# Kernel tuning notes

Hardware: AMD Instinct MI355X
Metric: run time of the kernel (lower is better)

Reference implementation:

```python
import jax, jax.numpy as jnp
import numpy as np

N = 8192          # nodes (atoms)
E = N * 20        # edges (avg 20 neighbors)
NG = 32           # graphs in batch
CUTOFF = 10.0
NBASIS = 40
NNEI = 20.0       # num_neighbors normalization
SQ2 = 0.5 ** 0.5


def _swish(x):
    return x * jax.nn.sigmoid(x)


def _radial(r, params):
    # Gaussian radial basis on [0, cutoff] followed by swish MLP 40->500->500->50->nweight
    centers = jnp.linspace(0.0, CUTOFF, NBASIS)
    width = centers[1] - centers[0]
    x = jnp.exp(-(((r[:, None] - centers) / width) ** 2))  # [E, NBASIS]
    w1, b1, w2, b2, w3, b3, w4, b4 = params
    x = _swish(x @ w1 + b1)
    x = _swish(x @ w2 + b2)
    x = _swish(x @ w3 + b3)
    return x @ w4 + b4


def setup_inputs() -> dict:
    key = jax.random.key(0)
    ks = jax.random.split(key, 12)
    z = jax.random.randint(ks[0], (N,), 0, 100)
    pos = jax.random.normal(ks[1], (N, 3), dtype=jnp.float32) * 2.0
    batch = jnp.sort(jax.random.randint(ks[2], (N,), 0, NG))
    edge_index = jax.random.randint(ks[3], (2, E), 0, N)

    def mlp_params(kk, dout):
        dims = [NBASIS, 500, 500, 50, dout]
        keys = jax.random.split(kk, len(dims) - 1)
        out = []
        for i, (a, b) in enumerate(zip(dims[:-1], dims[1:])):
            out.append(jax.random.normal(keys[i], (a, b), jnp.float32) / jnp.sqrt(a))
            out.append(jnp.zeros((b,), jnp.float32))
        return out

    rm1 = mlp_params(ks[4], 30 * 40 + 30 * 10)  # tp weights: 0x0->0 and 0x1->1 paths
    rm2 = mlp_params(ks[5], 30 * 1 + 10 * 1)    # tp weights: 0x0->0 and 1x1->0 paths
    inp = {
        'pos': pos,
        'emb': jax.random.normal(ks[6], (100, 30), jnp.float32),
        'si1_w': jax.random.normal(ks[7], (30, 40), jnp.float32),
        'si2_w': jax.random.normal(ks[8], (30, 1), jnp.float32),
    }
    names1 = ['rm1_w1', 'rm1_b1', 'rm1_w2', 'rm1_b2', 'rm1_w3', 'rm1_b3', 'rm1_w4', 'rm1_b4']
    names2 = ['rm2_w1', 'rm2_b1', 'rm2_w2', 'rm2_b2', 'rm2_w3', 'rm2_b3', 'rm2_w4', 'rm2_b4']
    inp.update(dict(zip(names1, rm1)))
    inp.update(dict(zip(names2, rm2)))
    inp['z'] = z
    inp['edge_index'] = edge_index
    inp['batch'] = batch
    return inp


def _forward(pos, emb, si1_w, si2_w, rm1, rm2, z, edge_index, batch):
    n = pos.shape[0]
    h = emb[z]                                  # [N, 30] embedding of atomic number
    row, col = edge_index[0], edge_index[1]
    edge_vec = pos[row] - pos[col]              # [E, 3]
    r = jnp.sqrt(jnp.sum(edge_vec ** 2, axis=1) + 1e-12)
    unit = edge_vec / r[:, None]
    # spherical harmonics (component norm): l=0 -> 1, l=1 -> sqrt(3)*unit; scaled by 1/sqrt(num_neighbors)
    sh = jnp.concatenate([jnp.ones_like(r)[:, None], jnp.sqrt(3.0) * unit], 1) / jnp.sqrt(NNEI)  # [E,4]
    e = edge_vec.shape[0]

    # ---- layer 1 Conv: (30,0,+) -> (40,0,+) + (10,1,-) ----
    s = h @ si1_w / jnp.sqrt(30.0)                                   # self-interaction, scalar block
    s_full = jnp.concatenate([s, jnp.zeros((n, 30), s.dtype)], 1)    # l=1 block has no input -> 0
    w = _radial(r, rm1)                                              # [E, 1500] per-edge tp weights
    w00 = w[:, :1200].reshape(e, 30, 40)
    w01 = w[:, 1200:].reshape(e, 30, 10)
    xj = h[row]
    m0 = jnp.einsum('eu,euv->ev', xj, w00) * sh[:, :1] / jnp.sqrt(30.0)                        # [E,40]
    m1 = jnp.einsum('eu,euv->ev', xj, w01)[:, :, None] * sh[:, None, 1:4] / jnp.sqrt(30.0)     # [E,10,3]
    msg = jnp.concatenate([m0, m1.reshape(e, 30)], 1)                # [E,70]
    agg = jax.ops.segment_sum(msg, col, num_segments=n)
    mask1 = jnp.concatenate([jnp.ones(40), jnp.zeros(30)]).astype(h.dtype)  # si output mask
    h1 = SQ2 * s_full + (1.0 + (SQ2 - 1.0) * mask1) * agg            # [N,70]

    # ---- gated block: swish on scalars, sigmoid gates on l=1 vectors ----
    scalars = _swish(h1[:, :30])
    gates = jax.nn.sigmoid(h1[:, 30:40])
    nons = h1[:, 40:70].reshape(n, 10, 3) * gates[:, :, None]
    h2 = jnp.concatenate([scalars, nons.reshape(n, 30)], 1)          # [N,60]

    # ---- final Conv: (30,0,+)+(10,1,-) -> (1,0,+)+(1,0,-) ----
    s2 = h2[:, :30] @ si2_w / jnp.sqrt(30.0)                         # [N,1]
    s2_full = jnp.concatenate([s2, jnp.zeros((n, 1), s2.dtype)], 1)
    w2 = _radial(r, rm2)                                             # [E,40]
    xj2 = h2[row]
    m0a = jnp.sum(xj2[:, :30] * w2[:, :30], axis=1) * sh[:, 0] / jnp.sqrt(30.0)
    dot = jnp.einsum('eum,em->eu', xj2[:, 30:].reshape(e, 10, 3), sh[:, 1:4]) / jnp.sqrt(3.0)  # 1x1->0 CG
    m0b = jnp.sum(dot * w2[:, 30:40], axis=1) / jnp.sqrt(10.0)
    msg2 = jnp.stack([m0a + m0b, jnp.zeros_like(m0a)], 1)            # (0,-1) output has no tp path
    agg2 = jax.ops.segment_sum(msg2, col, num_segments=n)
    mask2 = jnp.array([1.0, 0.0], h.dtype)
    hf = SQ2 * s2_full + (1.0 + (SQ2 - 1.0) * mask2) * agg2
    node_out = hf[:, 0] + hf[:, 1] ** 2
    return jax.ops.segment_sum(node_out[:, None], batch, num_segments=NG)  # [NG, 1]


def reference(pos, emb, si1_w, si2_w, rm1_w1, rm1_b1, rm1_w2, rm1_b2, rm1_w3, rm1_b3, rm1_w4, rm1_b4, rm2_w1, rm2_b1, rm2_w2, rm2_b2, rm2_w3, rm2_b3, rm2_w4, rm2_b4, z, edge_index, batch):
    rm1 = (rm1_w1, rm1_b1, rm1_w2, rm1_b2, rm1_w3, rm1_b3, rm1_w4, rm1_b4)
    rm2 = (rm2_w1, rm2_b1, rm2_w2, rm2_b2, rm2_w3, rm2_b3, rm2_w4, rm2_b4)
    return _forward(pos, emb, si1_w, si2_w, rm1, rm2, z, edge_index, batch)
```

## Files before the change

### kernel.cpp

```cpp
#include <hip/hip_runtime.h>
#include <stdint.h>

typedef __attribute__((ext_vector_type(8))) short bf16x8;
typedef __attribute__((ext_vector_type(4))) float f32x4;

#define N_NODES 8192
#define E_EDGES 163840
#define NGRAPH  32

#define INV_SQRT30 0.18257419f
#define SH0C       0.22360680f
#define SQRT3C     1.73205081f
#define INV_SQRT3  0.57735027f
#define INV_SQRT10 0.31622777f
#define SQ2C       0.70710678f

enum : unsigned {
  OFF_W1P1 = 0u,       OFF_W2P1 = 65536u,   OFF_W3P1 = 589824u,  OFF_W4P1 = 655360u,
  OFF_W1P2 = 851968u,  OFF_W2P2 = 917504u,  OFF_W3P2 = 1441792u, OFF_W4P2 = 1507328u,
  OFF_B1P1 = 1515520u, OFF_B2P1 = 1517568u, OFF_B3P1 = 1519616u, OFF_B4P1 = 1519872u,
  OFF_B1P2 = 1526016u, OFF_B2P2 = 1528064u, OFF_B3P2 = 1530112u, OFF_B4P2 = 1530368u,
  OFF_HN   = 1530624u,
  OFF_H2   = 2579200u,
  OFF_AGG  = 4676352u,
  OFF_AGG2 = 6970112u,
  OFF_GSUM = 7002880u,
  OFF_ZEND = 7003008u,
  OFF_SHL  = 7003136u,
  OFF_BAS  = 8969216u,
  OFF_W4N1 = 29940736u,
  OFF_X3   = 30186496u
};

__device__ __forceinline__ uint16_t f2bf(float f){
  union { float f; uint32_t u; } v; v.f = f;
  uint32_t r = v.u + 0x7fffu + ((v.u >> 16) & 1u);
  return (uint16_t)(r >> 16);
}
__device__ __forceinline__ float swishf(float x){ return x / (1.f + __expf(-x)); }
__device__ __forceinline__ float swish_fast(float x){
  float d = 1.f + __expf(-x);
  return x * __builtin_amdgcn_rcpf(d);
}

__device__ __forceinline__ void pack_mat(const float* __restrict__ src, int K, int N, int NP,
                                         uint16_t* __restrict__ dst, int t)
{
  int lane = t & 63;
  int tile = t >> 6;
  int NT = NP >> 4;
  int nn = tile % NT, kk = tile / NT;
  int k0 = kk*32 + ((lane >> 4) << 3);
  int n  = nn*16 + (lane & 15);
  union { short s[8]; bf16x8 v; } tmp;
#pragma unroll
  for (int b = 0; b < 8; ++b) {
    int k = k0 + b;
    tmp.s[b] = (k < K && n < N) ? (short)f2bf(src[(size_t)k*N + n]) : (short)0;
  }
  *reinterpret_cast<bf16x8*>(dst + (size_t)t*8) = tmp.v;
}

__device__ __forceinline__ void pack_w4n(const float* __restrict__ w4, const float* __restrict__ b4,
                                         uint16_t* __restrict__ dst, int t)
{
  int lane = t & 63;
  int tile = t >> 6;
  int u = tile >> 3, j = tile & 7;
  int kk = j >> 2, nn = j & 3;
  int k0 = kk*32 + ((lane >> 4) << 3);
  int n  = nn*16 + (lane & 15);
  union { short s[8]; bf16x8 v; } tmp;
#pragma unroll
  for (int b = 0; b < 8; ++b) {
    int k = k0 + b;
    float val = 0.f;
    if (n < 50) {
      int cg = (n < 40) ? (u*40 + n) : (1200 + u*10 + (n - 40));
      if (k < 50) val = w4[(size_t)k*1500 + cg];
      else if (k == 63) val = b4[cg];
    }
    tmp.s[b] = (short)f2bf(val);
  }
  *reinterpret_cast<bf16x8*>(dst + (size_t)t*8) = tmp.v;
}

__global__ void prep_kernel(const float* w1a, const float* w2a, const float* w3a, const float* w4a,
                            const float* w1b, const float* w2b, const float* w3b, const float* w4b,
                            const float* b1a, const float* b2a, const float* b3a, const float* b4a,
                            const float* b1b, const float* b2b, const float* b3b, const float* b4b,
                            const float* emb, const int* z, char* ws)
{
  int t = blockIdx.x * 256 + threadIdx.x;
  if      (t < 4096)   pack_mat(w1a, 40, 500, 512,  (uint16_t*)(ws + OFF_W1P1), t);
  else if (t < 36864)  pack_mat(w2a, 500,500, 512,  (uint16_t*)(ws + OFF_W2P1), t - 4096);
  else if (t < 40960)  pack_mat(w3a, 500, 50, 64,   (uint16_t*)(ws + OFF_W3P1), t - 36864);
  else if (t < 45056)  {  }
  else if (t < 49152)  pack_mat(w1b, 40, 500, 512,  (uint16_t*)(ws + OFF_W1P2), t - 45056);
  else if (t < 81920)  pack_mat(w2b, 500,500, 512,  (uint16_t*)(ws + OFF_W2P2), t - 49152);
  else if (t < 86016)  pack_mat(w3b, 500, 50, 64,   (uint16_t*)(ws + OFF_W3P2), t - 81920);
  else if (t < 86528)  pack_mat(w4b, 50,  40, 64,   (uint16_t*)(ws + OFF_W4P2), t - 86016);
  else if (t < 90304) {
    int loc = t - 86528;
    const float* src; float* dst; int realN;
    if      (loc < 512)  { src=b1a; dst=(float*)(ws+OFF_B1P1); realN=500; }
    else if (loc < 1024) { src=b2a; dst=(float*)(ws+OFF_B2P1); realN=500;  loc -= 512;  }
    else if (loc < 1088) { src=b3a; dst=(float*)(ws+OFF_B3P1); realN=50;   loc -= 1024; }
    else if (loc < 2624) { src=b4a; dst=(float*)(ws+OFF_B4P1); realN=1500; loc -= 1088; }
    else if (loc < 3136) { src=b1b; dst=(float*)(ws+OFF_B1P2); realN=500;  loc -= 2624; }
    else if (loc < 3648) { src=b2b; dst=(float*)(ws+OFF_B2P2); realN=500;  loc -= 3136; }
    else if (loc < 3712) { src=b3b; dst=(float*)(ws+OFF_B3P2); realN=50;   loc -= 3648; }
    else                 { src=b4b; dst=(float*)(ws+OFF_B4P2); realN=40;   loc -= 3712; }
    dst[loc] = (loc < realN) ? src[loc] : 0.f;
  }
  else if (t < 352448) {
    int i = t - 90304;
    int n = i >> 5, u = i & 31;
    float v = 0.f;
    if (u < 30) v = emb[(size_t)z[n]*30 + u] * INV_SQRT30;
    ((float*)(ws + OFF_HN))[i] = v;
  }
  else if (t < 367808) {
    pack_w4n(w4a, b4a, (uint16_t*)(ws + OFF_W4N1), t - 352448);
  }
}

__global__ void edge_meta(const float* __restrict__ pos, const int* __restrict__ eidx,
                          uint16_t* __restrict__ basis, float* __restrict__ shl)
{
  int e = blockIdx.x * 256 + threadIdx.x;
  if (e >= E_EDGES) return;
  int rn = eidx[e], cn = eidx[E_EDGES + e];
  float ax = pos[rn*3+0] - pos[cn*3+0];
  float ay = pos[rn*3+1] - pos[cn*3+1];
  float az = pos[rn*3+2] - pos[cn*3+2];
  float rr = sqrtf(ax*ax + ay*ay + az*az + 1e-12f);
  float s = SQRT3C * SH0C / rr;
  shl[e*3+0] = ax*s; shl[e*3+1] = ay*s; shl[e*3+2] = az*s;
#pragma unroll
  for (int j = 0; j < 8; ++j) {
    union { short s[8]; bf16x8 v; } tmp;
#pragma unroll
    for (int b = 0; b < 8; ++b) {
      int c = j*8 + b;
      float vv = 0.f;
      if (c < 40) { float t = rr*3.9f - (float)c; vv = __expf(-t*t); }
      tmp.s[b] = (short)f2bf(vv);
    }
    *reinterpret_cast<bf16x8*>(basis + (size_t)e*64 + j*8) = tmp.v;
  }
}

__global__ __launch_bounds__(512, 2)
void fused_mlp(const uint16_t* __restrict__ basis,
               const uint16_t* __restrict__ W1p, const float* __restrict__ b1,
               const uint16_t* __restrict__ W2p, const float* __restrict__ b2,
               const uint16_t* __restrict__ W3p, const float* __restrict__ b3,
               uint16_t* __restrict__ x3)
{
  __shared__ __align__(16) char actb[65536];

  const int tid = threadIdx.x, lane = tid & 63, wv = tid >> 6;
  const int m0 = blockIdx.x * 64;
  const int r = lane & 15, q = lane >> 4;

  const bf16x8* __restrict__ W1v = (const bf16x8*)W1p;
  const bf16x8* __restrict__ W2v = (const bf16x8*)W2p;
  const bf16x8* __restrict__ W3v = (const bf16x8*)W3p;

  f32x4 zv = {0.f, 0.f, 0.f, 0.f};
  const int colb2 = (wv*64 + r)*2;

  {
    f32x4 acc[4][4];
#pragma unroll
    for (int a = 0; a < 4; ++a)
#pragma unroll
      for (int c = 0; c < 4; ++c) acc[a][c] = zv;
#pragma unroll
    for (int ks = 0; ks < 2; ++ks) {
      bf16x8 af[4];
#pragma unroll
      for (int rb = 0; rb < 4; ++rb) {
        int row = m0 + rb*16 + r;
        af[rb] = *reinterpret_cast<const bf16x8*>((const char*)basis + (size_t)row*128 + ks*64 + q*16);
      }
      bf16x8 bfr[4];
#pragma unroll
      for (int j = 0; j < 4; ++j)
        bfr[j] = W1v[(size_t)((ks*32 + wv*4 + j)*64 + lane)];
#pragma unroll
      for (int j = 0; j < 4; ++j)
#pragma unroll
        for (int rb = 0; rb < 4; ++rb)
          acc[rb][j] = __builtin_amdgcn_mfma_f32_16x16x32_bf16(af[rb], bfr[j], acc[rb][j], 0, 0, 0);
    }
    float bsv[4];
#pragma unroll
    for (int nt = 0; nt < 4; ++nt) bsv[nt] = b1[wv*64 + nt*16 + r];
#pragma unroll
    for (int rb = 0; rb < 4; ++rb)
#pragma unroll
      for (int i = 0; i < 4; ++i) {
        int row = rb*16 + q*4 + i;
        int rowbase = row*1024;
        int mask = (row & 7) << 4;
#pragma unroll
        for (int nt = 0; nt < 4; ++nt)
          *(uint16_t*)(&actb[rowbase + ((colb2 + nt*32) ^ mask)]) = f2bf(swish_fast(acc[rb][nt][i] + bsv[nt]));
      }
  }
  __syncthreads();

  {
    f32x4 acc[4][4];
#pragma unroll
    for (int a = 0; a < 4; ++a)
#pragma unroll
      for (int c = 0; c < 4; ++c) acc[a][c] = zv;

    bf16x8 bnx[4];
#pragma unroll
    for (int j = 0; j < 4; ++j)
      bnx[j] = W2v[(size_t)((wv*4 + j)*64 + lane)];

#pragma unroll 1
    for (int ks = 0; ks < 16; ++ks) {
      bf16x8 bcur[4];
#pragma unroll
      for (int j = 0; j < 4; ++j) bcur[j] = bnx[j];
      if (ks + 1 < 16) {
#pragma unroll
        for (int j = 0; j < 4; ++j)
          bnx[j] = W2v[(size_t)(((ks + 1)*32 + wv*4 + j)*64 + lane)];
      }
      bf16x8 af[4];
#pragma unroll
      for (int rb = 0; rb < 4; ++rb) {
        int row = rb*16 + r;
        int off = row*1024 + ((ks*64 + q*16) ^ ((row & 7) << 4));
        af[rb] = *reinterpret_cast<const bf16x8*>(&actb[off]);
      }
#pragma unroll
      for (int j = 0; j < 4; ++j)
#pragma unroll
        for (int rb = 0; rb < 4; ++rb)
          acc[rb][j] = __builtin_amdgcn_mfma_f32_16x16x32_bf16(af[rb], bcur[j], acc[rb][j], 0, 0, 0);
    }
    __syncthreads();
    float bsv[4];
#pragma unroll
    for (int nt = 0; nt < 4; ++nt) bsv[nt] = b2[wv*64 + nt*16 + r];
#pragma unroll
    for (int rb = 0; rb < 4; ++rb)
#pragma unroll
      for (int i = 0; i < 4; ++i) {
        int row = rb*16 + q*4 + i;
        int rowbase = row*1024;
        int mask = (row & 7) << 4;
#pragma unroll
        for (int nt = 0; nt < 4; ++nt)
          *(uint16_t*)(&actb[rowbase + ((colb2 + nt*32) ^ mask)]) = f2bf(swish_fast(acc[rb][nt][i] + bsv[nt]));
      }
  }
  __syncthreads();

  {
    const int rb3 = wv >> 1, ntp = (wv & 1)*2;
    f32x4 acc[2];
    acc[0] = zv; acc[1] = zv;

    bf16x8 bnx[2];
#pragma unroll
    for (int j = 0; j < 2; ++j)
      bnx[j] = W3v[(size_t)((ntp + j)*64 + lane)];

#pragma unroll 1
    for (int ks = 0; ks < 16; ++ks) {
      bf16x8 bcur[2];
      bcur[0] = bnx[0]; bcur[1] = bnx[1];
      if (ks + 1 < 16) {
#pragma unroll
        for (int j = 0; j < 2; ++j)
          bnx[j] = W3v[(size_t)(((ks + 1)*4 + ntp + j)*64 + lane)];
      }
      int row = rb3*16 + r;
      int off = row*1024 + ((ks*64 + q*16) ^ ((row & 7) << 4));
      bf16x8 a = *reinterpret_cast<const bf16x8*>(&actb[off]);
#pragma unroll
      for (int j = 0; j < 2; ++j)
        acc[j] = __builtin_amdgcn_mfma_f32_16x16x32_bf16(a, bcur[j], acc[j], 0, 0, 0);
    }
#pragma unroll
    for (int j = 0; j < 2; ++j) {
      int col = (ntp + j)*16 + r;
      float bs = b3[col];
#pragma unroll
      for (int i = 0; i < 4; ++i) {
        int row = m0 + rb3*16 + q*4 + i;
        float v = swish_fast(acc[j][i] + bs);
        if (col == 63) v = 1.f;
        x3[(size_t)row*64 + col] = f2bf(v);
      }
    }
  }
}

__global__ __launch_bounds__(512, 4)
void tp1_gemm(const uint16_t* __restrict__ x3, const char* __restrict__ ws,
              const int* __restrict__ eidx, float* __restrict__ agg)
{
  __shared__ __align__(16) uint16_t Wst[2][4096];
  __shared__ float xjs[64*32];
  __shared__ float mbuf[64*64];
  __shared__ float shls[64*3];
  __shared__ int   rowl[64];
  __shared__ int   coll[64];

  const float* hN  = (const float*)(ws + OFF_HN);
  const float* shl = (const float*)(ws + OFF_SHL);
  const char*  W4n = (const char*)(ws + OFF_W4N1);

  const int tid = threadIdx.x, lane = tid & 63, wv = tid >> 6;
  const int e0l = blockIdx.x * 64;
  const int r_ = lane & 15, q_ = lane >> 4;
  const int rowg = wv >> 1, colg = wv & 1;

  if (tid < 64) { rowl[tid] = eidx[e0l + tid]; coll[tid] = eidx[E_EDGES + e0l + tid]; }
  for (int i = tid; i < 192; i += 512) shls[i] = shl[(size_t)e0l*3 + i];
  __syncthreads();
  for (int i = tid; i < 64*32; i += 512) {
    int e = i >> 5, u = i & 31;
    xjs[i] = hN[(size_t)rowl[e]*32 + u];
  }

  bf16x8 a0, a1;
  {
    int row = e0l + rowg*16 + r_;
    const char* base = (const char*)x3 + (size_t)row*128 + q_*16;
    a0 = *reinterpret_cast<const bf16x8*>(base);
    a1 = *reinterpret_cast<const bf16x8*>(base + 64);
  }

  const char* srcW = W4n + ((size_t)(tid >> 6)*64 + lane)*16;
  auto stageW = [&](int buf, int u) {
    __builtin_amdgcn_global_load_lds((const __attribute__((address_space(1))) void*)(srcW + (size_t)u*8192),
        (__attribute__((address_space(3))) void*)(&Wst[buf][(size_t)tid*8]), 16, 0, 0);
  };

  f32x4 zv = {0.f, 0.f, 0.f, 0.f};
  f32x4 accF[2];
  accF[0] = zv; accF[1] = zv;

  stageW(0, 0);
  __syncthreads();

  const char* wb0 = (const char*)&Wst[0][0] + ((size_t)(colg*2)*64 + lane)*16;
  const char* wb1 = (const char*)&Wst[1][0] + ((size_t)(colg*2)*64 + lane)*16;

  int cur = 0;
#pragma unroll 1
  for (int u = 0; u < 30; ++u) {
    if (u + 1 < 30) stageW(cur ^ 1, u + 1);
    const char* wb = cur ? wb1 : wb0;
    bf16x8 b00 = *reinterpret_cast<const bf16x8*>(wb);
    bf16x8 b01 = *reinterpret_cast<const bf16x8*>(wb + 1024);
    bf16x8 b10 = *reinterpret_cast<const bf16x8*>(wb + 4096);
    bf16x8 b11 = *reinterpret_cast<const bf16x8*>(wb + 5120);
    f32x4 t0 = __builtin_amdgcn_mfma_f32_16x16x32_bf16(a0, b00, zv, 0, 0, 0);
    t0 = __builtin_amdgcn_mfma_f32_16x16x32_bf16(a1, b10, t0, 0, 0, 0);
    f32x4 t1 = __builtin_amdgcn_mfma_f32_16x16x32_bf16(a0, b01, zv, 0, 0, 0);
    t1 = __builtin_amdgcn_mfma_f32_16x16x32_bf16(a1, b11, t1, 0, 0, 0);
#pragma unroll
    for (int i = 0; i < 4; ++i) {
      float xv = xjs[(rowg*16 + q_*4 + i)*32 + u];
      accF[0][i] += xv * t0[i];
      accF[1][i] += xv * t1[i];
    }
    if (u + 1 < 30) {
      asm volatile("s_waitcnt vmcnt(0)" ::: "memory");
      __builtin_amdgcn_s_barrier();
      cur ^= 1;
    }
  }

#pragma unroll
  for (int nt = 0; nt < 2; ++nt)
#pragma unroll
    for (int i = 0; i < 4; ++i)
      mbuf[(rowg*16 + q_*4 + i)*64 + colg*32 + nt*16 + r_] = accF[nt][i];
  __syncthreads();

#pragma unroll 1
  for (int i = tid; i < 64*70; i += 512) {
    int e = i/70, c = i - e*70;
    float v;
    if (c < 40) v = mbuf[e*64 + c] * SH0C;
    else { int vv = (c - 40)/3, k = (c - 40) - vv*3; v = mbuf[e*64 + 40 + vv] * shls[e*3 + k]; }
    atomicAdd(&agg[(size_t)coll[e]*70 + c], v);
  }
}

__global__ __launch_bounds__(512, 2)
void tp2_kernel(const uint16_t* __restrict__ x3, const char* __restrict__ ws,
                const int* __restrict__ eidx, float* __restrict__ agg2)
{
  constexpr int P2 = 67;
  __shared__ float wbuf2[64 * P2];
  __shared__ float xjs[64*30];
  __shared__ float xjv[64*30];
  __shared__ float Db[64*10];
  __shared__ float shls[64*3];
  __shared__ int   rowl[64];
  __shared__ int   coll[64];

  const float* h2  = (const float*)(ws + OFF_H2);
  const float* shl = (const float*)(ws + OFF_SHL);
  const float* b4p = (const float*)(ws + OFF_B4P2);
  const bf16x8* __restrict__ bv4 = (const bf16x8*)(ws + OFF_W4P2);

  const int tid = threadIdx.x, lane = tid & 63, wv = tid >> 6;
  const int e0l = blockIdx.x * 64;
  const int r_ = lane & 15, q_ = lane >> 4;

  if (tid < 64) { rowl[tid] = eidx[e0l + tid]; coll[tid] = eidx[E_EDGES + e0l + tid]; }
  for (int i = tid; i < 192; i += 512) shls[i] = shl[(size_t)e0l*3 + i];
  __syncthreads();
  for (int i = tid; i < 64*60; i += 512) {
    int e = i/60, u = i - e*60;
    float v = h2[(size_t)rowl[e]*64 + u];
    if (u < 30) xjs[e*30 + u] = v; else xjv[e*30 + (u - 30)] = v;
  }
  __syncthreads();
  for (int i = tid; i < 640; i += 512) {
    int e = i/10, v = i - e*10;
    float d = 0.f;
#pragma unroll
    for (int m = 0; m < 3; ++m) d += xjv[e*30 + v*3 + m] * shls[e*3 + m];
    Db[i] = d * INV_SQRT3;
  }

  const int rbase = (wv >> 2)*2, nt4 = wv & 3;
  bf16x8 a4[2][2];
#pragma unroll
  for (int kk = 0; kk < 2; ++kk)
#pragma unroll
    for (int rbi = 0; rbi < 2; ++rbi) {
      int row = e0l + (rbase + rbi)*16 + r_;
      a4[kk][rbi] = *reinterpret_cast<const bf16x8*>((const char*)x3 + (size_t)row*128 + kk*64 + q_*16);
    }
  f32x4 acc[2];
  f32x4 zv = {0.f, 0.f, 0.f, 0.f};
  acc[0] = zv; acc[1] = zv;
#pragma unroll
  for (int kk = 0; kk < 2; ++kk) {
    bf16x8 b4 = bv4[(size_t)(kk*4 + nt4)*64 + lane];
#pragma unroll
    for (int rbi = 0; rbi < 2; ++rbi)
      acc[rbi] = __builtin_amdgcn_mfma_f32_16x16x32_bf16(a4[kk][rbi], b4, acc[rbi], 0, 0, 0);
  }
  __syncthreads();
  {
    int cg = nt4*16 + r_;
    float bs = b4p[cg];
#pragma unroll
    for (int rbi = 0; rbi < 2; ++rbi)
#pragma unroll
      for (int i2 = 0; i2 < 4; ++i2) {
        int e = (rbase + rbi)*16 + q_*4 + i2;
        wbuf2[e*P2 + cg] = acc[rbi][i2] + bs;
      }
  }
  __syncthreads();

  if (tid < 64) {
    int e = tid;
    float m = 0.f, m2 = 0.f;
#pragma unroll
    for (int c = 0; c < 30; ++c) m += xjs[e*30 + c] * wbuf2[e*P2 + c];
#pragma unroll
    for (int vv = 0; vv < 10; ++vv) m2 += Db[e*10 + vv] * wbuf2[e*P2 + 30 + vv];
    atomicAdd(&agg2[coll[e]], m * (SH0C * INV_SQRT30) + m2 * INV_SQRT10);
  }
}

__global__ void node_mid(char* ws, const float* __restrict__ si1w)
{
  int nid = blockIdx.x * blockDim.x + threadIdx.x;
  if (nid >= N_NODES) return;
  const float* hN  = (const float*)(ws + OFF_HN)  + (size_t)nid*32;
  const float* agg = (const float*)(ws + OFF_AGG) + (size_t)nid*70;
  float* h2        = (float*)(ws + OFF_H2)        + (size_t)nid*64;

  float hn[30];
#pragma unroll
  for (int u = 0; u < 30; ++u) hn[u] = hN[u];

  float h1[70];
#pragma unroll 1
  for (int v = 0; v < 40; ++v) {
    float s = 0.f;
#pragma unroll
    for (int u = 0; u < 30; ++u) s += hn[u] * si1w[u*40 + v];
    h1[v] = SQ2C * (s + agg[v]);
  }
#pragma unroll
  for (int c = 40; c < 70; ++c) h1[c] = agg[c];

#pragma unroll
  for (int u = 0; u < 30; ++u) h2[u] = swishf(h1[u]);
#pragma unroll
  for (int v = 0; v < 10; ++v) {
    float g = 1.f / (1.f + __expf(-h1[30 + v]));
#pragma unroll
    for (int k = 0; k < 3; ++k) h2[30 + v*3 + k] = h1[40 + v*3 + k] * g;
  }
}

__global__ void node_final(char* ws, const float* __restrict__ si2w, const int* __restrict__ batch)
{
  __shared__ float ls[NGRAPH];
  if (threadIdx.x < NGRAPH) ls[threadIdx.x] = 0.f;
  __syncthreads();
  int nid = blockIdx.x * blockDim.x + threadIdx.x;
  if (nid < N_NODES) {
    const float* h2   = (const float*)(ws + OFF_H2) + (size_t)nid*64;
    const float* agg2 = (const float*)(ws + OFF_AGG2);
    float s2 = 0.f;
#pragma unroll
    for (int u = 0; u < 30; ++u) s2 += h2[u] * si2w[u];
    float val = SQ2C * (s2 * INV_SQRT30 + agg2[nid]);
    atomicAdd(&ls[batch[nid]], val);
  }
  __syncthreads();
  if (threadIdx.x < NGRAPH)
    atomicAdd(((float*)(ws + OFF_GSUM)) + threadIdx.x, ls[threadIdx.x]);
}

__global__ void write_out(const char* ws, float* out)
{
  int g = threadIdx.x;
  if (g < NGRAPH) out[g] = ((const float*)(ws + OFF_GSUM))[g];
}

extern "C" void kernel_launch(void* const* d_in, const int* in_sizes, int n_in,
                              void* d_out, int out_size, void* d_ws, size_t ws_size,
                              hipStream_t stream)
{
  const float* pos  = (const float*)d_in[0];
  const float* emb  = (const float*)d_in[1];
  const float* si1w = (const float*)d_in[2];
  const float* si2w = (const float*)d_in[3];
  const float* w1a = (const float*)d_in[4];  const float* b1a = (const float*)d_in[5];
  const float* w2a = (const float*)d_in[6];  const float* b2a = (const float*)d_in[7];
  const float* w3a = (const float*)d_in[8];  const float* b3a = (const float*)d_in[9];
  const float* w4a = (const float*)d_in[10]; const float* b4a = (const float*)d_in[11];
  const float* w1b = (const float*)d_in[12]; const float* b1b = (const float*)d_in[13];
  const float* w2b = (const float*)d_in[14]; const float* b2b = (const float*)d_in[15];
  const float* w3b = (const float*)d_in[16]; const float* b3b = (const float*)d_in[17];
  const float* w4b = (const float*)d_in[18]; const float* b4b = (const float*)d_in[19];
  const int* z     = (const int*)d_in[20];
  const int* eidx  = (const int*)d_in[21];
  const int* batch = (const int*)d_in[22];
  char* ws = (char*)d_ws;

  uint16_t* basis = (uint16_t*)(ws + OFF_BAS);
  float*    shl   = (float*)(ws + OFF_SHL);
  uint16_t* x3    = (uint16_t*)(ws + OFF_X3);

  hipMemsetAsync(ws + OFF_AGG, 0, OFF_ZEND - OFF_AGG, stream);

  prep_kernel<<<1437, 256, 0, stream>>>(w1a, w2a, w3a, w4a, w1b, w2b, w3b, w4b,
                                        b1a, b2a, b3a, b4a, b1b, b2b, b3b, b4b,
                                        emb, z, ws);
  edge_meta<<<E_EDGES/256, 256, 0, stream>>>(pos, eidx, basis, shl);

  fused_mlp<<<E_EDGES/64, 512, 0, stream>>>(basis,
      (const uint16_t*)(ws + OFF_W1P1), (const float*)(ws + OFF_B1P1),
      (const uint16_t*)(ws + OFF_W2P1), (const float*)(ws + OFF_B2P1),
      (const uint16_t*)(ws + OFF_W3P1), (const float*)(ws + OFF_B3P1), x3);
  tp1_gemm<<<E_EDGES/64, 512, 0, stream>>>(x3, ws, eidx, (float*)(ws + OFF_AGG));

  node_mid<<<N_NODES/256, 256, 0, stream>>>(ws, si1w);

  fused_mlp<<<E_EDGES/64, 512, 0, stream>>>(basis,
      (const uint16_t*)(ws + OFF_W1P2), (const float*)(ws + OFF_B1P2),
      (const uint16_t*)(ws + OFF_W2P2), (const float*)(ws + OFF_B2P2),
      (const uint16_t*)(ws + OFF_W3P2), (const float*)(ws + OFF_B3P2), x3);
  tp2_kernel<<<E_EDGES/64, 512, 0, stream>>>(x3, ws, eidx, (float*)(ws + OFF_AGG2));

  node_final<<<N_NODES/256, 256, 0, stream>>>(ws, si2w, batch);
  write_out<<<1, 64, 0, stream>>>(ws, (float*)d_out);
}
```

Baseline: 532.9 us.

## Halve MLP edge tile to 32 rows and drop LDS weight staging in tp1

The fused MLP kernel now processes 32 edges per block instead of 64. This halves its LDS footprint and accumulator registers and doubles the grid, and the explicit software prefetch of W2/W3 fragments is replaced by direct loads in loops unrolled by two. The tp1 kernel drops its double-buffered global_load_lds weight staging and per-iteration barriers and reads the weights directly from global/L2, with launch bounds lowered to 2 blocks per CU. The intent is higher occupancy and fewer synchronisations, at the cost of half the weight reuse per block in the MLP (twice the weight traffic) and unstaged global weight reads in tp1.

```diff
diff --git a/kernel.cpp b/kernel.cpp
--- a/kernel.cpp
+++ b/kernel.cpp
@@ -158,10 +158,10 @@
                const uint16_t* __restrict__ W3p, const float* __restrict__ b3,
                uint16_t* __restrict__ x3)
 {
-  __shared__ __align__(16) char actb[65536];
+  __shared__ __align__(16) char actb[32768];
 
   const int tid = threadIdx.x, lane = tid & 63, wv = tid >> 6;
-  const int m0 = blockIdx.x * 64;
+  const int m0 = blockIdx.x * 32;
   const int r = lane & 15, q = lane >> 4;
 
   const bf16x8* __restrict__ W1v = (const bf16x8*)W1p;
@@ -172,16 +172,16 @@
   const int colb2 = (wv*64 + r)*2;
 
   {
-    f32x4 acc[4][4];
-#pragma unroll
-    for (int a = 0; a < 4; ++a)
+    f32x4 acc[2][4];
+#pragma unroll
+    for (int a = 0; a < 2; ++a)
 #pragma unroll
       for (int c = 0; c < 4; ++c) acc[a][c] = zv;
 #pragma unroll
     for (int ks = 0; ks < 2; ++ks) {
-      bf16x8 af[4];
-#pragma unroll
-      for (int rb = 0; rb < 4; ++rb) {
+      bf16x8 af[2];
+#pragma unroll
+      for (int rb = 0; rb < 2; ++rb) {
         int row = m0 + rb*16 + r;
         af[rb] = *reinterpret_cast<const bf16x8*>((const char*)basis + (size_t)row*128 + ks*64 + q*16);
       }
@@ -192,14 +192,14 @@
 #pragma unroll
       for (int j = 0; j < 4; ++j)
 #pragma unroll
-        for (int rb = 0; rb < 4; ++rb)
+        for (int rb = 0; rb < 2; ++rb)
           acc[rb][j] = __builtin_amdgcn_mfma_f32_16x16x32_bf16(af[rb], bfr[j], acc[rb][j], 0, 0, 0);
     }
     float bsv[4];
 #pragma unroll
     for (int nt = 0; nt < 4; ++nt) bsv[nt] = b1[wv*64 + nt*16 + r];
 #pragma unroll
-    for (int rb = 0; rb < 4; ++rb)
+    for (int rb = 0; rb < 2; ++rb)
 #pragma unroll
       for (int i = 0; i < 4; ++i) {
         int row = rb*16 + q*4 + i;
@@ -213,46 +213,36 @@
   __syncthreads();
 
   {
-    f32x4 acc[4][4];
-#pragma unroll
-    for (int a = 0; a < 4; ++a)
+    f32x4 acc[2][4];
+#pragma unroll
+    for (int a = 0; a < 2; ++a)
 #pragma unroll
       for (int c = 0; c < 4; ++c) acc[a][c] = zv;
-
-    bf16x8 bnx[4];
-#pragma unroll
-    for (int j = 0; j < 4; ++j)
-      bnx[j] = W2v[(size_t)((wv*4 + j)*64 + lane)];
-
-#pragma unroll 1
+#pragma unroll 2
     for (int ks = 0; ks < 16; ++ks) {
-      bf16x8 bcur[4];
-#pragma unroll
-      for (int j = 0; j < 4; ++j) bcur[j] = bnx[j];
-      if (ks + 1 < 16) {
-#pragma unroll
-        for (int j = 0; j < 4; ++j)
-          bnx[j] = W2v[(size_t)(((ks + 1)*32 + wv*4 + j)*64 + lane)];
-      }
-      bf16x8 af[4];
-#pragma unroll
-      for (int rb = 0; rb < 4; ++rb) {
+      bf16x8 af[2];
+#pragma unroll
+      for (int rb = 0; rb < 2; ++rb) {
         int row = rb*16 + r;
         int off = row*1024 + ((ks*64 + q*16) ^ ((row & 7) << 4));
         af[rb] = *reinterpret_cast<const bf16x8*>(&actb[off]);
       }
+      bf16x8 bfr[4];
 #pragma unroll
       for (int j = 0; j < 4; ++j)
-#pragma unroll
-        for (int rb = 0; rb < 4; ++rb)
-          acc[rb][j] = __builtin_amdgcn_mfma_f32_16x16x32_bf16(af[rb], bcur[j], acc[rb][j], 0, 0, 0);
+        bfr[j] = W2v[(size_t)((ks*32 + wv*4 + j)*64 + lane)];
+#pragma unroll
+      for (int j = 0; j < 4; ++j)
+#pragma unroll
+        for (int rb = 0; rb < 2; ++rb)
+          acc[rb][j] = __builtin_amdgcn_mfma_f32_16x16x32_bf16(af[rb], bfr[j], acc[rb][j], 0, 0, 0);
     }
     __syncthreads();
     float bsv[4];
 #pragma unroll
     for (int nt = 0; nt < 4; ++nt) bsv[nt] = b2[wv*64 + nt*16 + r];
 #pragma unroll
-    for (int rb = 0; rb < 4; ++rb)
+    for (int rb = 0; rb < 2; ++rb)
 #pragma unroll
       for (int i = 0; i < 4; ++i) {
         int row = rb*16 + q*4 + i;
@@ -266,51 +256,32 @@
   __syncthreads();
 
   {
-    const int rb3 = wv >> 1, ntp = (wv & 1)*2;
-    f32x4 acc[2];
-    acc[0] = zv; acc[1] = zv;
-
-    bf16x8 bnx[2];
-#pragma unroll
-    for (int j = 0; j < 2; ++j)
-      bnx[j] = W3v[(size_t)((ntp + j)*64 + lane)];
-
-#pragma unroll 1
+    const int rb3 = wv >> 2, nt3 = wv & 3;
+    f32x4 acc1 = zv;
+#pragma unroll 2
     for (int ks = 0; ks < 16; ++ks) {
-      bf16x8 bcur[2];
-      bcur[0] = bnx[0]; bcur[1] = bnx[1];
-      if (ks + 1 < 16) {
-#pragma unroll
-        for (int j = 0; j < 2; ++j)
-          bnx[j] = W3v[(size_t)(((ks + 1)*4 + ntp + j)*64 + lane)];
-      }
       int row = rb3*16 + r;
       int off = row*1024 + ((ks*64 + q*16) ^ ((row & 7) << 4));
       bf16x8 a = *reinterpret_cast<const bf16x8*>(&actb[off]);
-#pragma unroll
-      for (int j = 0; j < 2; ++j)
-        acc[j] = __builtin_amdgcn_mfma_f32_16x16x32_bf16(a, bcur[j], acc[j], 0, 0, 0);
-    }
-#pragma unroll
-    for (int j = 0; j < 2; ++j) {
-      int col = (ntp + j)*16 + r;
-      float bs = b3[col];
-#pragma unroll
-      for (int i = 0; i < 4; ++i) {
-        int row = m0 + rb3*16 + q*4 + i;
-        float v = swish_fast(acc[j][i] + bs);
-        if (col == 63) v = 1.f;
-        x3[(size_t)row*64 + col] = f2bf(v);
-      }
-    }
-  }
-}
-
-__global__ __launch_bounds__(512, 4)
+      bf16x8 bb = W3v[(size_t)((ks*4 + nt3)*64 + lane)];
+      acc1 = __builtin_amdgcn_mfma_f32_16x16x32_bf16(a, bb, acc1, 0, 0, 0);
+    }
+    int col = nt3*16 + r;
+    float bs = b3[col];
+#pragma unroll
+    for (int i = 0; i < 4; ++i) {
+      int row = m0 + rb3*16 + q*4 + i;
+      float v = swish_fast(acc1[i] + bs);
+      if (col == 63) v = 1.f;
+      x3[(size_t)row*64 + col] = f2bf(v);
+    }
+  }
+}
+
+__global__ __launch_bounds__(512, 2)
 void tp1_gemm(const uint16_t* __restrict__ x3, const char* __restrict__ ws,
               const int* __restrict__ eidx, float* __restrict__ agg)
 {
-  __shared__ __align__(16) uint16_t Wst[2][4096];
   __shared__ float xjs[64*32];
   __shared__ float mbuf[64*64];
   __shared__ float shls[64*3];
@@ -319,7 +290,7 @@
 
   const float* hN  = (const float*)(ws + OFF_HN);
   const float* shl = (const float*)(ws + OFF_SHL);
-  const char*  W4n = (const char*)(ws + OFF_W4N1);
+  const bf16x8* __restrict__ Wv = (const bf16x8*)(ws + OFF_W4N1);
 
   const int tid = threadIdx.x, lane = tid & 63, wv = tid >> 6;
   const int e0l = blockIdx.x * 64;
@@ -341,32 +312,20 @@
     a0 = *reinterpret_cast<const bf16x8*>(base);
     a1 = *reinterpret_cast<const bf16x8*>(base + 64);
   }
-
-  const char* srcW = W4n + ((size_t)(tid >> 6)*64 + lane)*16;
-  auto stageW = [&](int buf, int u) {
-    __builtin_amdgcn_global_load_lds((const __attribute__((address_space(1))) void*)(srcW + (size_t)u*8192),
-        (__attribute__((address_space(3))) void*)(&Wst[buf][(size_t)tid*8]), 16, 0, 0);
-  };
+  __syncthreads();
 
   f32x4 zv = {0.f, 0.f, 0.f, 0.f};
   f32x4 accF[2];
   accF[0] = zv; accF[1] = zv;
 
-  stageW(0, 0);
-  __syncthreads();
-
-  const char* wb0 = (const char*)&Wst[0][0] + ((size_t)(colg*2)*64 + lane)*16;
-  const char* wb1 = (const char*)&Wst[1][0] + ((size_t)(colg*2)*64 + lane)*16;
-
-  int cur = 0;
-#pragma unroll 1
+  const size_t wbase = (size_t)(colg*2)*64 + lane;
+
+#pragma unroll 2
   for (int u = 0; u < 30; ++u) {
-    if (u + 1 < 30) stageW(cur ^ 1, u + 1);
-    const char* wb = cur ? wb1 : wb0;
-    bf16x8 b00 = *reinterpret_cast<const bf16x8*>(wb);
-    bf16x8 b01 = *reinterpret_cast<const bf16x8*>(wb + 1024);
-    bf16x8 b10 = *reinterpret_cast<const bf16x8*>(wb + 4096);
-    bf16x8 b11 = *reinterpret_cast<const bf16x8*>(wb + 5120);
+    bf16x8 b00 = Wv[(size_t)(u*8 + 0)*64 + wbase];
+    bf16x8 b01 = Wv[(size_t)(u*8 + 1)*64 + wbase];
+    bf16x8 b10 = Wv[(size_t)(u*8 + 4)*64 + wbase];
+    bf16x8 b11 = Wv[(size_t)(u*8 + 5)*64 + wbase];
     f32x4 t0 = __builtin_amdgcn_mfma_f32_16x16x32_bf16(a0, b00, zv, 0, 0, 0);
     t0 = __builtin_amdgcn_mfma_f32_16x16x32_bf16(a1, b10, t0, 0, 0, 0);
     f32x4 t1 = __builtin_amdgcn_mfma_f32_16x16x32_bf16(a0, b01, zv, 0, 0, 0);
@@ -376,11 +335,6 @@
       float xv = xjs[(rowg*16 + q_*4 + i)*32 + u];
       accF[0][i] += xv * t0[i];
       accF[1][i] += xv * t1[i];
-    }
-    if (u + 1 < 30) {
-      asm volatile("s_waitcnt vmcnt(0)" ::: "memory");
-      __builtin_amdgcn_s_barrier();
-      cur ^= 1;
     }
   }
 
@@ -575,7 +529,7 @@
                                         emb, z, ws);
   edge_meta<<<E_EDGES/256, 256, 0, stream>>>(pos, eidx, basis, shl);
 
-  fused_mlp<<<E_EDGES/64, 512, 0, stream>>>(basis,
+  fused_mlp<<<E_EDGES/32, 512, 0, stream>>>(basis,
       (const uint16_t*)(ws + OFF_W1P1), (const float*)(ws + OFF_B1P1),
       (const uint16_t*)(ws + OFF_W2P1), (const float*)(ws + OFF_B2P1),
       (const uint16_t*)(ws + OFF_W3P1), (const float*)(ws + OFF_B3P1), x3);
@@ -583,7 +537,7 @@
 
   node_mid<<<N_NODES/256, 256, 0, stream>>>(ws, si1w);
 
-  fused_mlp<<<E_EDGES/64, 512, 0, stream>>>(basis,
+  fused_mlp<<<E_EDGES/32, 512, 0, stream>>>(basis,
       (const uint16_t*)(ws + OFF_W1P2), (const float*)(ws + OFF_B1P2),
       (const uint16_t*)(ws + OFF_W2P2), (const float*)(ws + OFF_B2P2),
       (const uint16_t*)(ws + OFF_W3P2), (const float*)(ws + OFF_B3P2), x3);
```

Result: no change. 527.0 us (-1.1%).

## Use 32x32 MFMA for layer-2 GEMM and load tp1 weights directly from global

Applied to the files above, without the earlier changes.

The 500x500 hidden layer of the radial MLP now uses 32x32x16 bf16 MFMA tiles, with the weights repacked into a matching 32-column fragment layout and the register prefetch double-buffer replaced by direct loads in a loop unrolled by two. Larger tiles mean fewer LDS activation reads per MFMA. Separately, tp1_gemm drops its LDS weight staging and per-iteration barriers, reads weight fragments straight from global memory and cache, and lowers its occupancy hint from 4 to 2. The trade-off is more exposed global-load latency in exchange for fewer barriers and less LDS use.

```diff
diff --git a/kernel.cpp b/kernel.cpp
--- a/kernel.cpp
+++ b/kernel.cpp
@@ -3,6 +3,7 @@
 
 typedef __attribute__((ext_vector_type(8))) short bf16x8;
 typedef __attribute__((ext_vector_type(4))) float f32x4;
+typedef __attribute__((ext_vector_type(16))) float f32x16;
 
 #define N_NODES 8192
 #define E_EDGES 163840
@@ -61,6 +62,24 @@
   *reinterpret_cast<bf16x8*>(dst + (size_t)t*8) = tmp.v;
 }
 
+__device__ __forceinline__ void pack_mat32(const float* __restrict__ src, int K, int N, int NP,
+                                           uint16_t* __restrict__ dst, int t)
+{
+  int lane = t & 63;
+  int tile = t >> 6;
+  int NT = NP >> 5;
+  int nn = tile % NT, kk = tile / NT;
+  int k0 = kk*16 + ((lane >> 5) << 3);
+  int n  = nn*32 + (lane & 31);
+  union { short s[8]; bf16x8 v; } tmp;
+#pragma unroll
+  for (int b = 0; b < 8; ++b) {
+    int k = k0 + b;
+    tmp.s[b] = (k < K && n < N) ? (short)f2bf(src[(size_t)k*N + n]) : (short)0;
+  }
+  *reinterpret_cast<bf16x8*>(dst + (size_t)t*8) = tmp.v;
+}
+
 __device__ __forceinline__ void pack_w4n(const float* __restrict__ w4, const float* __restrict__ b4,
                                          uint16_t* __restrict__ dst, int t)
 {
@@ -93,11 +112,11 @@
 {
   int t = blockIdx.x * 256 + threadIdx.x;
   if      (t < 4096)   pack_mat(w1a, 40, 500, 512,  (uint16_t*)(ws + OFF_W1P1), t);
-  else if (t < 36864)  pack_mat(w2a, 500,500, 512,  (uint16_t*)(ws + OFF_W2P1), t - 4096);
+  else if (t < 36864)  pack_mat32(w2a, 500,500, 512, (uint16_t*)(ws + OFF_W2P1), t - 4096);
   else if (t < 40960)  pack_mat(w3a, 500, 50, 64,   (uint16_t*)(ws + OFF_W3P1), t - 36864);
   else if (t < 45056)  {  }
   else if (t < 49152)  pack_mat(w1b, 40, 500, 512,  (uint16_t*)(ws + OFF_W1P2), t - 45056);
-  else if (t < 81920)  pack_mat(w2b, 500,500, 512,  (uint16_t*)(ws + OFF_W2P2), t - 49152);
+  else if (t < 81920)  pack_mat32(w2b, 500,500, 512, (uint16_t*)(ws + OFF_W2P2), t - 49152);
   else if (t < 86016)  pack_mat(w3b, 500, 50, 64,   (uint16_t*)(ws + OFF_W3P2), t - 81920);
   else if (t < 86528)  pack_mat(w4b, 50,  40, 64,   (uint16_t*)(ws + OFF_W4P2), t - 86016);
   else if (t < 90304) {
@@ -163,6 +182,7 @@
   const int tid = threadIdx.x, lane = tid & 63, wv = tid >> 6;
   const int m0 = blockIdx.x * 64;
   const int r = lane & 15, q = lane >> 4;
+  const int r32 = lane & 31, q32 = lane >> 5;
 
   const bf16x8* __restrict__ W1v = (const bf16x8*)W1p;
   const bf16x8* __restrict__ W2v = (const bf16x8*)W2p;
@@ -213,54 +233,48 @@
   __syncthreads();
 
   {
-    f32x4 acc[4][4];
-#pragma unroll
-    for (int a = 0; a < 4; ++a)
-#pragma unroll
-      for (int c = 0; c < 4; ++c) acc[a][c] = zv;
-
-    bf16x8 bnx[4];
-#pragma unroll
-    for (int j = 0; j < 4; ++j)
-      bnx[j] = W2v[(size_t)((wv*4 + j)*64 + lane)];
-
-#pragma unroll 1
-    for (int ks = 0; ks < 16; ++ks) {
-      bf16x8 bcur[4];
-#pragma unroll
-      for (int j = 0; j < 4; ++j) bcur[j] = bnx[j];
-      if (ks + 1 < 16) {
-#pragma unroll
-        for (int j = 0; j < 4; ++j)
-          bnx[j] = W2v[(size_t)(((ks + 1)*32 + wv*4 + j)*64 + lane)];
-      }
-      bf16x8 af[4];
-#pragma unroll
-      for (int rb = 0; rb < 4; ++rb) {
-        int row = rb*16 + r;
-        int off = row*1024 + ((ks*64 + q*16) ^ ((row & 7) << 4));
+    f32x16 acc2[2][2];
+#pragma unroll
+    for (int a = 0; a < 2; ++a)
+#pragma unroll
+      for (int c = 0; c < 2; ++c)
+#pragma unroll
+        for (int g = 0; g < 16; ++g) acc2[a][c][g] = 0.f;
+
+#pragma unroll 2
+    for (int ks = 0; ks < 32; ++ks) {
+      bf16x8 af[2];
+#pragma unroll
+      for (int rb = 0; rb < 2; ++rb) {
+        int row = rb*32 + r32;
+        int off = row*1024 + (((ks*16 + q32*8)*2) ^ ((row & 7) << 4));
         af[rb] = *reinterpret_cast<const bf16x8*>(&actb[off]);
       }
-#pragma unroll
-      for (int j = 0; j < 4; ++j)
-#pragma unroll
-        for (int rb = 0; rb < 4; ++rb)
-          acc[rb][j] = __builtin_amdgcn_mfma_f32_16x16x32_bf16(af[rb], bcur[j], acc[rb][j], 0, 0, 0);
+      bf16x8 bfr[2];
+#pragma unroll
+      for (int ct = 0; ct < 2; ++ct)
+        bfr[ct] = W2v[(size_t)((ks*16 + wv*2 + ct)*64 + lane)];
+#pragma unroll
+      for (int ct = 0; ct < 2; ++ct)
+#pragma unroll
+        for (int rb = 0; rb < 2; ++rb)
+          acc2[rb][ct] = __builtin_amdgcn_mfma_f32_32x32x16_bf16(af[rb], bfr[ct], acc2[rb][ct], 0, 0, 0);
     }
     __syncthreads();
-    float bsv[4];
-#pragma unroll
-    for (int nt = 0; nt < 4; ++nt) bsv[nt] = b2[wv*64 + nt*16 + r];
-#pragma unroll
-    for (int rb = 0; rb < 4; ++rb)
-#pragma unroll
-      for (int i = 0; i < 4; ++i) {
-        int row = rb*16 + q*4 + i;
+    float bsv[2];
+#pragma unroll
+    for (int ct = 0; ct < 2; ++ct) bsv[ct] = b2[wv*64 + ct*32 + r32];
+    const int colb32 = (wv*64 + r32)*2;
+#pragma unroll
+    for (int rb = 0; rb < 2; ++rb)
+#pragma unroll
+      for (int g = 0; g < 16; ++g) {
+        int row = rb*32 + (g & 3) + 8*(g >> 2) + 4*q32;
         int rowbase = row*1024;
         int mask = (row & 7) << 4;
 #pragma unroll
-        for (int nt = 0; nt < 4; ++nt)
-          *(uint16_t*)(&actb[rowbase + ((colb2 + nt*32) ^ mask)]) = f2bf(swish_fast(acc[rb][nt][i] + bsv[nt]));
+        for (int ct = 0; ct < 2; ++ct)
+          *(uint16_t*)(&actb[rowbase + ((colb32 + ct*64) ^ mask)]) = f2bf(swish_fast(acc2[rb][ct][g] + bsv[ct]));
       }
   }
   __syncthreads();
@@ -306,11 +320,10 @@
   }
 }
 
-__global__ __launch_bounds__(512, 4)
+__global__ __launch_bounds__(512, 2)
 void tp1_gemm(const uint16_t* __restrict__ x3, const char* __restrict__ ws,
               const int* __restrict__ eidx, float* __restrict__ agg)
 {
-  __shared__ __align__(16) uint16_t Wst[2][4096];
   __shared__ float xjs[64*32];
   __shared__ float mbuf[64*64];
   __shared__ float shls[64*3];
@@ -319,7 +332,7 @@
 
   const float* hN  = (const float*)(ws + OFF_HN);
   const float* shl = (const float*)(ws + OFF_SHL);
-  const char*  W4n = (const char*)(ws + OFF_W4N1);
+  const bf16x8* __restrict__ Wv = (const bf16x8*)(ws + OFF_W4N1);
 
   const int tid = threadIdx.x, lane = tid & 63, wv = tid >> 6;
   const int e0l = blockIdx.x * 64;
@@ -341,32 +354,20 @@
     a0 = *reinterpret_cast<const bf16x8*>(base);
     a1 = *reinterpret_cast<const bf16x8*>(base + 64);
   }
-
-  const char* srcW = W4n + ((size_t)(tid >> 6)*64 + lane)*16;
-  auto stageW = [&](int buf, int u) {
-    __builtin_amdgcn_global_load_lds((const __attribute__((address_space(1))) void*)(srcW + (size_t)u*8192),
-        (__attribute__((address_space(3))) void*)(&Wst[buf][(size_t)tid*8]), 16, 0, 0);
-  };
+  __syncthreads();
 
   f32x4 zv = {0.f, 0.f, 0.f, 0.f};
   f32x4 accF[2];
   accF[0] = zv; accF[1] = zv;
 
-  stageW(0, 0);
-  __syncthreads();
-
-  const char* wb0 = (const char*)&Wst[0][0] + ((size_t)(colg*2)*64 + lane)*16;
-  const char* wb1 = (const char*)&Wst[1][0] + ((size_t)(colg*2)*64 + lane)*16;
-
-  int cur = 0;
-#pragma unroll 1
+  const size_t wbase = (size_t)(colg*2)*64 + lane;
+
+#pragma unroll 2
   for (int u = 0; u < 30; ++u) {
-    if (u + 1 < 30) stageW(cur ^ 1, u + 1);
-    const char* wb = cur ? wb1 : wb0;
-    bf16x8 b00 = *reinterpret_cast<const bf16x8*>(wb);
-    bf16x8 b01 = *reinterpret_cast<const bf16x8*>(wb + 1024);
-    bf16x8 b10 = *reinterpret_cast<const bf16x8*>(wb + 4096);
-    bf16x8 b11 = *reinterpret_cast<const bf16x8*>(wb + 5120);
+    bf16x8 b00 = Wv[(size_t)(u*8 + 0)*64 + wbase];
+    bf16x8 b01 = Wv[(size_t)(u*8 + 1)*64 + wbase];
+    bf16x8 b10 = Wv[(size_t)(u*8 + 4)*64 + wbase];
+    bf16x8 b11 = Wv[(size_t)(u*8 + 5)*64 + wbase];
     f32x4 t0 = __builtin_amdgcn_mfma_f32_16x16x32_bf16(a0, b00, zv, 0, 0, 0);
     t0 = __builtin_amdgcn_mfma_f32_16x16x32_bf16(a1, b10, t0, 0, 0, 0);
     f32x4 t1 = __builtin_amdgcn_mfma_f32_16x16x32_bf16(a0, b01, zv, 0, 0, 0);
@@ -376,11 +377,6 @@
       float xv = xjs[(rowg*16 + q_*4 + i)*32 + u];
       accF[0][i] += xv * t0[i];
       accF[1][i] += xv * t1[i];
-    }
-    if (u + 1 < 30) {
-      asm volatile("s_waitcnt vmcnt(0)" ::: "memory");
-      __builtin_amdgcn_s_barrier();
-      cur ^= 1;
     }
   }
 
```

After: 547.6 us. 2.8% more time.
